# Performance work log

Measured on AMD Instinct MI355X. Metric: run time of the kernel, lower is better.

## Reference

```python
import jax, jax.numpy as jnp
import numpy as np

TEMPERATURE = 0.5
EPS = 1e-8  # F.cosine_similarity eps


def _neg_mask_indices(B):
    # mask: ones, zero diagonal, zero the two positive off-diagonals
    N = 2 * B
    mask = np.ones((N, N), dtype=bool)
    np.fill_diagonal(mask, False)
    idx = np.arange(B)
    mask[idx, idx + B] = False
    mask[idx + B, idx] = False
    rows, cols = np.nonzero(mask)  # static, computed at trace time
    return rows, cols


def setup_inputs() -> dict:
    key = jax.random.key(0)
    k1, k2 = jax.random.split(key)
    B, D = 4096, 128
    z_i = jax.random.normal(k1, (B, D), dtype=jnp.float32)
    z_j = jax.random.normal(k2, (B, D), dtype=jnp.float32)
    return {"z_i": z_i, "z_j": z_j}


def reference(z_i, z_j):
    B = z_i.shape[0]
    N = 2 * B
    z = jnp.concatenate([z_i, z_j], axis=0)  # [N, D]
    norm = jnp.maximum(jnp.linalg.norm(z, axis=1, keepdims=True), EPS)
    zn = z / norm
    sim = (zn @ zn.T) / TEMPERATURE  # [N, N] cosine similarity / temp

    # positives: the i <-> i+B pairs
    sim_i_j = jnp.diagonal(sim, offset=B)
    sim_j_i = jnp.diagonal(sim, offset=-B)
    positives = jnp.concatenate([sim_i_j, sim_j_i], axis=0)[:, None]  # [N, 1]

    rows, cols = _neg_mask_indices(B)
    negatives = sim[rows, cols].reshape(N, N - 2)  # [N, N-2]

    logits = jnp.concatenate([positives, negatives], axis=1)  # [N, N-1]
    # cross-entropy with labels == 0 (positive is column 0)
    loss = jnp.mean(jax.nn.logsumexp(logits, axis=1) - logits[:, 0])
    return loss
```

## Files before the change

### kernel.cpp

```cpp
#include <hip/hip_runtime.h>
#include <hip/hip_bf16.h>
#include <math.h>


typedef __attribute__((ext_vector_type(8))) short bf16x8;
typedef __attribute__((ext_vector_type(4))) float f32x4;

#define NROWS 8192
#define DDIM  128
#define BHALF 4096
#define NCG   8
#define CGSZ  1024
#define CHUNKC 128
#define NPH   8
#define SQRT_E2S 1.6986435980707531f
#define LN2      0.6931471805599453f
#define EXPDIAG  7.38905609893065f

static __device__ __forceinline__ unsigned short f2bf(float f) {
  unsigned int u = __float_as_uint(f);
  unsigned int r = (u + 0x7fffu + ((u >> 16) & 1u)) >> 16;
  return (unsigned short)r;
}

static __device__ __forceinline__ void glds16(const unsigned short* g, unsigned short* l) {
  __builtin_amdgcn_global_load_lds((const __attribute__((address_space(1))) unsigned int*)g,
                                   (__attribute__((address_space(3))) unsigned int*)l,
                                   16, 0, 0);
}

__global__ void norm_kernel(const float* __restrict__ zi, const float* __restrict__ zj,
                            unsigned short* __restrict__ zn,
                            float* __restrict__ pos, float* __restrict__ out) {
  __shared__ float2 xbuf[2][64];
  int wave = threadIdx.x >> 6;
  int lane = threadIdx.x & 63;
  int pi   = blockIdx.x * 2 + (wave & 1);
  int row  = pi + (wave >> 1) * BHALF;
  const float* src = (row < BHALF) ? (zi + (size_t)row * DDIM)
                                   : (zj + (size_t)(row - BHALF) * DDIM);
  float2 v = *(const float2*)(src + 2 * lane);
  float ss = v.x * v.x + v.y * v.y;
  #pragma unroll
  for (int off = 1; off < 64; off <<= 1) ss += __shfl_xor(ss, off);
  float scale = SQRT_E2S / fmaxf(sqrtf(ss), 1e-8f);
  v.x *= scale; v.y *= scale;
  unsigned int lo = f2bf(v.x), hi = f2bf(v.y);
  ((unsigned int*)(zn + (size_t)row * DDIM))[lane] = lo | (hi << 16);

  if (wave >= 2) xbuf[wave - 2][lane] = v;
  __syncthreads();
  if (wave < 2) {
    float2 w = xbuf[wave][lane];
    float d = v.x * w.x + v.y * w.y;
    #pragma unroll
    for (int off = 1; off < 64; off <<= 1) d += __shfl_xor(d, off);
    if (lane == 0) pos[pi] = d;
  }
  if (blockIdx.x == 0 && threadIdx.x == 0) out[0] = 0.0f;
}

__global__ __launch_bounds__(256, 2)
void sim_kernel(const unsigned short* __restrict__ zn, float* __restrict__ part) {
  __shared__ unsigned short lds[2 * CHUNKC * DDIM];

  const int w    = threadIdx.x >> 6;
  const int lane = threadIdx.x & 63;
  const int l15  = lane & 15;
  const int quad = lane >> 4;

  const int strip = blockIdx.x >> 3;
  const int cg    = blockIdx.x & 7;
  const int row_base = strip * 128 + w * 32;
  const int col0     = cg * CGSZ;

  bf16x8 a[2][4];
  const unsigned short* abase = zn + (size_t)(row_base + l15) * DDIM + quad * 8;
  #pragma unroll
  for (int mi = 0; mi < 2; ++mi)
    #pragma unroll
    for (int kf = 0; kf < 4; ++kf)
      a[mi][kf] = *(const bf16x8*)(abase + mi * 16 * DDIM + kf * 32);
  __builtin_amdgcn_sched_barrier(0);

  const int rq = lane >> 4;
  const int cl = lane & 15;

#define STAGE(CH, BUF)                                                         \
  {                                                                            \
    _Pragma("unroll")                                                          \
    for (int i = 0; i < 8; ++i) {                                              \
      int r = (w * 8 + i) * 4 + rq;                                            \
      int c = cl ^ (r & 15);                                                   \
      glds16(zn + (size_t)(col0 + (CH) * CHUNKC + r) * DDIM + c * 8,           \
             lds + (BUF) * (CHUNKC * DDIM) + (w * 8 + i) * 512);               \
    }                                                                          \
  }

  STAGE(0, 0)
  STAGE(1, 1)
  __builtin_amdgcn_sched_barrier(0);

  int rdoff[4];
  #pragma unroll
  for (int kf = 0; kf < 4; ++kf)
    rdoff[kf] = l15 * DDIM + (((quad + 4 * kf) ^ l15) << 3);

  float rs[2][4];
  #pragma unroll
  for (int mi = 0; mi < 2; ++mi)
    #pragma unroll
    for (int r = 0; r < 4; ++r) rs[mi][r] = 0.0f;

#define COMPUTE(LB)                                                            \
  {                                                                            \
    _Pragma("unroll")                                                          \
    for (int ni = 0; ni < 8; ++ni) {                                           \
      bf16x8 b[4];                                                             \
      _Pragma("unroll")                                                        \
      for (int kf = 0; kf < 4; ++kf)                                           \
        b[kf] = *(const bf16x8*)((LB) + ni * 16 * DDIM + rdoff[kf]);           \
      f32x4 z = {0.0f, 0.0f, 0.0f, 0.0f};                                      \
      f32x4 acc0 = __builtin_amdgcn_mfma_f32_16x16x32_bf16(a[0][0], b[0], z, 0, 0, 0); \
      f32x4 acc1 = __builtin_amdgcn_mfma_f32_16x16x32_bf16(a[1][0], b[0], z, 0, 0, 0); \
      _Pragma("unroll")                                                        \
      for (int kf = 1; kf < 4; ++kf) {                                         \
        acc0 = __builtin_amdgcn_mfma_f32_16x16x32_bf16(a[0][kf], b[kf], acc0, 0, 0, 0); \
        acc1 = __builtin_amdgcn_mfma_f32_16x16x32_bf16(a[1][kf], b[kf], acc1, 0, 0, 0); \
      }                                                                        \
      _Pragma("unroll")                                                        \
      for (int r = 0; r < 4; ++r) {                                            \
        rs[0][r] += __builtin_amdgcn_exp2f(acc0[r]);                           \
        rs[1][r] += __builtin_amdgcn_exp2f(acc1[r]);                           \
      }                                                                        \
    }                                                                          \
  }

  #pragma unroll 1
  for (int ch = 0; ch < 6; ++ch) {
    asm volatile("s_waitcnt vmcnt(8)" ::: "memory");
    __builtin_amdgcn_s_barrier();
    __builtin_amdgcn_sched_barrier(0);
    const unsigned short* lb = lds + (ch & 1) * (CHUNKC * DDIM);
    COMPUTE(lb)
    __builtin_amdgcn_sched_barrier(0);
    __builtin_amdgcn_s_barrier();
    STAGE(ch + 2, (ch & 1))
  }
  asm volatile("s_waitcnt vmcnt(8)" ::: "memory");
  __builtin_amdgcn_s_barrier();
  __builtin_amdgcn_sched_barrier(0);
  COMPUTE(lds)
  asm volatile("s_waitcnt vmcnt(0)" ::: "memory");
  __builtin_amdgcn_s_barrier();
  __builtin_amdgcn_sched_barrier(0);
  COMPUTE(lds + CHUNKC * DDIM)
#undef COMPUTE
#undef STAGE

  #pragma unroll
  for (int mi = 0; mi < 2; ++mi)
    #pragma unroll
    for (int r = 0; r < 4; ++r) {
      float v = rs[mi][r];
      v += __shfl_xor(v, 1);
      v += __shfl_xor(v, 2);
      v += __shfl_xor(v, 4);
      v += __shfl_xor(v, 8);
      if (l15 == 0)
        part[(size_t)cg * NROWS + row_base + mi * 16 + quad * 4 + r] = v;
    }
}

__global__ void finalize_kernel(const float* __restrict__ part,
                                const float* __restrict__ pos,
                                float* __restrict__ out) {
  __shared__ float red[4];
  int r = blockIdx.x * 256 + threadIdx.x;
  float s = 0.0f;
  #pragma unroll
  for (int k = 0; k < NCG; ++k) s += part[(size_t)k * NROWS + r];
  float v = logf(s - EXPDIAG) - LN2 * pos[r & (BHALF - 1)];
  #pragma unroll
  for (int off = 1; off < 64; off <<= 1) v += __shfl_xor(v, off);
  int wave = threadIdx.x >> 6, lane = threadIdx.x & 63;
  if (lane == 0) red[wave] = v;
  __syncthreads();
  if (threadIdx.x == 0)
    atomicAdd(out, (red[0] + red[1] + red[2] + red[3]) * (1.0f / 8192.0f));
}

extern "C" void kernel_launch(void* const* d_in, const int* in_sizes, int n_in,
                              void* d_out, int out_size, void* d_ws, size_t ws_size,
                              hipStream_t stream) {
  const float* zi = (const float*)d_in[0];
  const float* zj = (const float*)d_in[1];
  char* ws = (char*)d_ws;
  unsigned short* zn = (unsigned short*)ws;
  float* part = (float*)(ws + (size_t)NROWS * DDIM * 2);
  float* pos  = (float*)(ws + (size_t)NROWS * DDIM * 2
                            + (size_t)NCG * NROWS * 4);
  float* out = (float*)d_out;

  norm_kernel<<<2048, 256, 0, stream>>>(zi, zj, zn, pos, out);
  sim_kernel<<<512, 256, 0, stream>>>(zn, part);
  finalize_kernel<<<32, 256, 0, stream>>>(part, pos, out);
}
```

Baseline: 81.80 us.

## Fuse normalize, similarity and finalize into one persistent kernel with grid barriers

Merges the three launches into a single 512-block kernel that normalizes rows, waits at a software grid barrier, runs the MFMA similarity/exp-sum pass, waits again, and then does the final log-sum reduction. This removes two kernel launch gaps and the tail drain between stages. The positive dot product is now computed from the fp32 pair in the same wave. The change relies on all 512 blocks being co-resident (2 per CU) for the spin barrier to avoid deadlock. It also adds a memset of the barrier counters plus atomic spin overhead.

```diff
diff --git a/kernel.cpp b/kernel.cpp
--- a/kernel.cpp
+++ b/kernel.cpp
@@ -12,7 +12,7 @@
 #define NCG   8
 #define CGSZ  1024
 #define CHUNKC 128
-#define NPH   8
+#define NBLK  512
 #define SQRT_E2S 1.6986435980707531f
 #define LN2      0.6931471805599453f
 #define EXPDIAG  7.38905609893065f
@@ -29,39 +29,23 @@
                                    16, 0, 0);
 }
 
-__global__ void norm_kernel(const float* __restrict__ zi, const float* __restrict__ zj,
-                            unsigned short* __restrict__ zn,
-                            float* __restrict__ pos, float* __restrict__ out) {
-  __shared__ float2 xbuf[2][64];
-  int wave = threadIdx.x >> 6;
-  int lane = threadIdx.x & 63;
-  int pi   = blockIdx.x * 2 + (wave & 1);
-  int row  = pi + (wave >> 1) * BHALF;
-  const float* src = (row < BHALF) ? (zi + (size_t)row * DDIM)
-                                   : (zj + (size_t)(row - BHALF) * DDIM);
-  float2 v = *(const float2*)(src + 2 * lane);
-  float ss = v.x * v.x + v.y * v.y;
-  #pragma unroll
-  for (int off = 1; off < 64; off <<= 1) ss += __shfl_xor(ss, off);
-  float scale = SQRT_E2S / fmaxf(sqrtf(ss), 1e-8f);
-  v.x *= scale; v.y *= scale;
-  unsigned int lo = f2bf(v.x), hi = f2bf(v.y);
-  ((unsigned int*)(zn + (size_t)row * DDIM))[lane] = lo | (hi << 16);
-
-  if (wave >= 2) xbuf[wave - 2][lane] = v;
+static __device__ __forceinline__ void grid_barrier(unsigned int* c) {
+  __threadfence();
   __syncthreads();
-  if (wave < 2) {
-    float2 w = xbuf[wave][lane];
-    float d = v.x * w.x + v.y * w.y;
-    #pragma unroll
-    for (int off = 1; off < 64; off <<= 1) d += __shfl_xor(d, off);
-    if (lane == 0) pos[pi] = d;
-  }
-  if (blockIdx.x == 0 && threadIdx.x == 0) out[0] = 0.0f;
+  if (threadIdx.x == 0) {
+    __hip_atomic_fetch_add(c, 1u, __ATOMIC_ACQ_REL, __HIP_MEMORY_SCOPE_AGENT);
+    while (__hip_atomic_load(c, __ATOMIC_ACQUIRE, __HIP_MEMORY_SCOPE_AGENT) < NBLK)
+      __builtin_amdgcn_s_sleep(1);
+  }
+  __syncthreads();
+  __threadfence();
 }
 
 __global__ __launch_bounds__(256, 2)
-void sim_kernel(const unsigned short* __restrict__ zn, float* __restrict__ part) {
+void fused_kernel(const float* __restrict__ zi, const float* __restrict__ zj,
+                  unsigned short* __restrict__ zn, float* __restrict__ part,
+                  float* __restrict__ pos, unsigned int* __restrict__ ctr,
+                  float* __restrict__ out) {
   __shared__ unsigned short lds[2 * CHUNKC * DDIM];
 
   const int w    = threadIdx.x >> 6;
@@ -69,125 +53,157 @@
   const int l15  = lane & 15;
   const int quad = lane >> 4;
 
-  const int strip = blockIdx.x >> 3;
-  const int cg    = blockIdx.x & 7;
-  const int row_base = strip * 128 + w * 32;
-  const int col0     = cg * CGSZ;
-
-  bf16x8 a[2][4];
-  const unsigned short* abase = zn + (size_t)(row_base + l15) * DDIM + quad * 8;
   #pragma unroll
-  for (int mi = 0; mi < 2; ++mi)
+  for (int p = 0; p < 2; ++p) {
+    int pi = blockIdx.x * 8 + p * 4 + w;
+    float2 vi = *(const float2*)(zi + (size_t)pi * DDIM + 2 * lane);
+    float2 vj = *(const float2*)(zj + (size_t)pi * DDIM + 2 * lane);
+    float ssi = vi.x * vi.x + vi.y * vi.y;
+    float ssj = vj.x * vj.x + vj.y * vj.y;
+    float d   = vi.x * vj.x + vi.y * vj.y;
+    #pragma unroll
+    for (int off = 1; off < 64; off <<= 1) {
+      ssi += __shfl_xor(ssi, off);
+      ssj += __shfl_xor(ssj, off);
+      d   += __shfl_xor(d, off);
+    }
+    float si = SQRT_E2S / fmaxf(sqrtf(ssi), 1e-8f);
+    float sj = SQRT_E2S / fmaxf(sqrtf(ssj), 1e-8f);
+    unsigned int li = f2bf(vi.x * si), hi_ = f2bf(vi.y * si);
+    unsigned int lj = f2bf(vj.x * sj), hj  = f2bf(vj.y * sj);
+    ((unsigned int*)(zn + (size_t)pi * DDIM))[lane]           = li | (hi_ << 16);
+    ((unsigned int*)(zn + (size_t)(pi + BHALF) * DDIM))[lane] = lj | (hj << 16);
+    if (lane == 0) pos[pi] = d * si * sj;
+  }
+  if (blockIdx.x == 0 && threadIdx.x == 0) out[0] = 0.0f;
+
+  grid_barrier(&ctr[0]);
+
+  {
+    const int strip = blockIdx.x >> 3;
+    const int cg_   = blockIdx.x & 7;
+    const int row_base = strip * 128 + w * 32;
+    const int col0     = cg_ * CGSZ;
+
+    bf16x8 a[2][4];
+    const unsigned short* abase = zn + (size_t)(row_base + l15) * DDIM + quad * 8;
+    #pragma unroll
+    for (int mi = 0; mi < 2; ++mi)
+      #pragma unroll
+      for (int kf = 0; kf < 4; ++kf)
+        a[mi][kf] = *(const bf16x8*)(abase + mi * 16 * DDIM + kf * 32);
+    __builtin_amdgcn_sched_barrier(0);
+
+    const int rq = lane >> 4;
+    const int cl = lane & 15;
+
+#define STAGE(CH, BUF)                                                         \
+    {                                                                          \
+      _Pragma("unroll")                                                        \
+      for (int i = 0; i < 8; ++i) {                                            \
+        int r = (w * 8 + i) * 4 + rq;                                          \
+        int c = cl ^ (r & 15);                                                 \
+        glds16(zn + (size_t)(col0 + (CH) * CHUNKC + r) * DDIM + c * 8,         \
+               lds + (BUF) * (CHUNKC * DDIM) + (w * 8 + i) * 512);             \
+      }                                                                        \
+    }
+
+    STAGE(0, 0)
+    STAGE(1, 1)
+    __builtin_amdgcn_sched_barrier(0);
+
+    int rdoff[4];
     #pragma unroll
     for (int kf = 0; kf < 4; ++kf)
-      a[mi][kf] = *(const bf16x8*)(abase + mi * 16 * DDIM + kf * 32);
-  __builtin_amdgcn_sched_barrier(0);
-
-  const int rq = lane >> 4;
-  const int cl = lane & 15;
-
-#define STAGE(CH, BUF)                                                         \
-  {                                                                            \
-    _Pragma("unroll")                                                          \
-    for (int i = 0; i < 8; ++i) {                                              \
-      int r = (w * 8 + i) * 4 + rq;                                            \
-      int c = cl ^ (r & 15);                                                   \
-      glds16(zn + (size_t)(col0 + (CH) * CHUNKC + r) * DDIM + c * 8,           \
-             lds + (BUF) * (CHUNKC * DDIM) + (w * 8 + i) * 512);               \
-    }                                                                          \
-  }
-
-  STAGE(0, 0)
-  STAGE(1, 1)
-  __builtin_amdgcn_sched_barrier(0);
-
-  int rdoff[4];
-  #pragma unroll
-  for (int kf = 0; kf < 4; ++kf)
-    rdoff[kf] = l15 * DDIM + (((quad + 4 * kf) ^ l15) << 3);
-
-  float rs[2][4];
-  #pragma unroll
-  for (int mi = 0; mi < 2; ++mi)
-    #pragma unroll
-    for (int r = 0; r < 4; ++r) rs[mi][r] = 0.0f;
+      rdoff[kf] = l15 * DDIM + (((quad + 4 * kf) ^ l15) << 3);
+
+    float rs[2][4];
+    #pragma unroll
+    for (int mi = 0; mi < 2; ++mi)
+      #pragma unroll
+      for (int r = 0; r < 4; ++r) rs[mi][r] = 0.0f;
 
 #define COMPUTE(LB)                                                            \
-  {                                                                            \
-    _Pragma("unroll")                                                          \
-    for (int ni = 0; ni < 8; ++ni) {                                           \
-      bf16x8 b[4];                                                             \
+    {                                                                          \
       _Pragma("unroll")                                                        \
-      for (int kf = 0; kf < 4; ++kf)                                           \
-        b[kf] = *(const bf16x8*)((LB) + ni * 16 * DDIM + rdoff[kf]);           \
-      f32x4 z = {0.0f, 0.0f, 0.0f, 0.0f};                                      \
-      f32x4 acc0 = __builtin_amdgcn_mfma_f32_16x16x32_bf16(a[0][0], b[0], z, 0, 0, 0); \
-      f32x4 acc1 = __builtin_amdgcn_mfma_f32_16x16x32_bf16(a[1][0], b[0], z, 0, 0, 0); \
-      _Pragma("unroll")                                                        \
-      for (int kf = 1; kf < 4; ++kf) {                                         \
-        acc0 = __builtin_amdgcn_mfma_f32_16x16x32_bf16(a[0][kf], b[kf], acc0, 0, 0, 0); \
-        acc1 = __builtin_amdgcn_mfma_f32_16x16x32_bf16(a[1][kf], b[kf], acc1, 0, 0, 0); \
+      for (int ni = 0; ni < 8; ++ni) {                                         \
+        bf16x8 b[4];                                                           \
+        _Pragma("unroll")                                                      \
+        for (int kf = 0; kf < 4; ++kf)                                         \
+          b[kf] = *(const bf16x8*)((LB) + ni * 16 * DDIM + rdoff[kf]);         \
+        f32x4 z = {0.0f, 0.0f, 0.0f, 0.0f};                                    \
+        f32x4 acc0 = __builtin_amdgcn_mfma_f32_16x16x32_bf16(a[0][0], b[0], z, 0, 0, 0); \
+        f32x4 acc1 = __builtin_amdgcn_mfma_f32_16x16x32_bf16(a[1][0], b[0], z, 0, 0, 0); \
+        _Pragma("unroll")                                                      \
+        for (int kf = 1; kf < 4; ++kf) {                                       \
+          acc0 = __builtin_amdgcn_mfma_f32_16x16x32_bf16(a[0][kf], b[kf], acc0, 0, 0, 0); \
+          acc1 = __builtin_amdgcn_mfma_f32_16x16x32_bf16(a[1][kf], b[kf], acc1, 0, 0, 0); \
+        }                                                                      \
+        _Pragma("unroll")                                                      \
+        for (int r = 0; r < 4; ++r) {                                          \
+          rs[0][r] += __builtin_amdgcn_exp2f(acc0[r]);                         \
+          rs[1][r] += __builtin_amdgcn_exp2f(acc1[r]);                         \
+        }                                                                      \
       }                                                                        \
-      _Pragma("unroll")                                                        \
-      for (int r = 0; r < 4; ++r) {                                            \
-        rs[0][r] += __builtin_amdgcn_exp2f(acc0[r]);                           \
-        rs[1][r] += __builtin_amdgcn_exp2f(acc1[r]);                           \
-      }                                                                        \
-    }                                                                          \
-  }
-
-  #pragma unroll 1
-  for (int ch = 0; ch < 6; ++ch) {
+    }
+
+    #pragma unroll 1
+    for (int ch = 0; ch < 6; ++ch) {
+      asm volatile("s_waitcnt vmcnt(8)" ::: "memory");
+      __builtin_amdgcn_s_barrier();
+      __builtin_amdgcn_sched_barrier(0);
+      const unsigned short* lb = lds + (ch & 1) * (CHUNKC * DDIM);
+      COMPUTE(lb)
+      __builtin_amdgcn_sched_barrier(0);
+      __builtin_amdgcn_s_barrier();
+      STAGE(ch + 2, (ch & 1))
+    }
     asm volatile("s_waitcnt vmcnt(8)" ::: "memory");
     __builtin_amdgcn_s_barrier();
     __builtin_amdgcn_sched_barrier(0);
-    const unsigned short* lb = lds + (ch & 1) * (CHUNKC * DDIM);
-    COMPUTE(lb)
-    __builtin_amdgcn_sched_barrier(0);
+    COMPUTE(lds)
+    asm volatile("s_waitcnt vmcnt(0)" ::: "memory");
     __builtin_amdgcn_s_barrier();
-    STAGE(ch + 2, (ch & 1))
-  }
-  asm volatile("s_waitcnt vmcnt(8)" ::: "memory");
-  __builtin_amdgcn_s_barrier();
-  __builtin_amdgcn_sched_barrier(0);
-  COMPUTE(lds)
-  asm volatile("s_waitcnt vmcnt(0)" ::: "memory");
-  __builtin_amdgcn_s_barrier();
-  __builtin_amdgcn_sched_barrier(0);
-  COMPUTE(lds + CHUNKC * DDIM)
+    __builtin_amdgcn_sched_barrier(0);
+    COMPUTE(lds + CHUNKC * DDIM)
 #undef COMPUTE
 #undef STAGE
 
-  #pragma unroll
-  for (int mi = 0; mi < 2; ++mi)
-    #pragma unroll
-    for (int r = 0; r < 4; ++r) {
-      float v = rs[mi][r];
+    #pragma unroll
+    for (int mi = 0; mi < 2; ++mi)
+      #pragma unroll
+      for (int r = 0; r < 4; ++r) {
+        float v = rs[mi][r];
+        v += __shfl_xor(v, 1);
+        v += __shfl_xor(v, 2);
+        v += __shfl_xor(v, 4);
+        v += __shfl_xor(v, 8);
+        if (l15 == 0)
+          part[(size_t)cg_ * NROWS + row_base + mi * 16 + quad * 4 + r] = v;
+      }
+  }
+
+  grid_barrier(&ctr[1]);
+
+  {
+    float* fsum = (float*)lds;
+    int r = blockIdx.x * 16 + l15;
+    int k = (threadIdx.x >> 4);
+    float s = (k < NCG) ? part[(size_t)k * NROWS + r] : 0.0f;
+    s += __shfl_xor(s, 16);
+    s += __shfl_xor(s, 32);
+    if (lane < 16) fsum[w * 16 + lane] = s;
+    __syncthreads();
+    if (w == 0 && lane < 16) {
+      float tot = fsum[lane] + fsum[16 + lane] + fsum[32 + lane] + fsum[48 + lane];
+      float v = logf(tot - EXPDIAG) - LN2 * pos[r & (BHALF - 1)];
       v += __shfl_xor(v, 1);
       v += __shfl_xor(v, 2);
       v += __shfl_xor(v, 4);
       v += __shfl_xor(v, 8);
-      if (l15 == 0)
-        part[(size_t)cg * NROWS + row_base + mi * 16 + quad * 4 + r] = v;
-    }
-}
-
-__global__ void finalize_kernel(const float* __restrict__ part,
-                                const float* __restrict__ pos,
-                                float* __restrict__ out) {
-  __shared__ float red[4];
-  int r = blockIdx.x * 256 + threadIdx.x;
-  float s = 0.0f;
-  #pragma unroll
-  for (int k = 0; k < NCG; ++k) s += part[(size_t)k * NROWS + r];
-  float v = logf(s - EXPDIAG) - LN2 * pos[r & (BHALF - 1)];
-  #pragma unroll
-  for (int off = 1; off < 64; off <<= 1) v += __shfl_xor(v, off);
-  int wave = threadIdx.x >> 6, lane = threadIdx.x & 63;
-  if (lane == 0) red[wave] = v;
-  __syncthreads();
-  if (threadIdx.x == 0)
-    atomicAdd(out, (red[0] + red[1] + red[2] + red[3]) * (1.0f / 8192.0f));
+      if (lane == 0) atomicAdd(out, v * (1.0f / 8192.0f));
+    }
+  }
 }
 
 extern "C" void kernel_launch(void* const* d_in, const int* in_sizes, int n_in,
@@ -200,9 +216,11 @@
   float* part = (float*)(ws + (size_t)NROWS * DDIM * 2);
   float* pos  = (float*)(ws + (size_t)NROWS * DDIM * 2
                             + (size_t)NCG * NROWS * 4);
+  unsigned int* ctr = (unsigned int*)(ws + (size_t)NROWS * DDIM * 2
+                                         + (size_t)NCG * NROWS * 4
+                                         + (size_t)BHALF * 4);
   float* out = (float*)d_out;
 
-  norm_kernel<<<2048, 256, 0, stream>>>(zi, zj, zn, pos, out);
-  sim_kernel<<<512, 256, 0, stream>>>(zn, part);
-  finalize_kernel<<<32, 256, 0, stream>>>(part, pos, out);
-}
+  hipMemsetAsync(ctr, 0, 2 * sizeof(unsigned int), stream);
+  fused_kernel<<<NBLK, 256, 0, stream>>>(zi, zj, zn, part, pos, ctr, out);
+}
```

After: 276.6 us. 3.38x slower.
